# Performance work log

Hardware: AMD Instinct MI355X
Metric: run time of the kernel (lower is better)

Reference implementation:

```python
import jax, jax.numpy as jnp
import numpy as np

N, E, C, L, NG = 50000, 600000, 128, 7, 512
EPS = 1e-7


def layer_norm(z, g, b):
    mu = z.mean(-1, keepdims=True)
    var = ((z - mu) ** 2).mean(-1, keepdims=True)
    return (z - mu) * jax.lax.rsqrt(var + 1e-5) * g + b


def setup_inputs() -> dict:
    key = jax.random.key(0)
    ks = jax.random.split(key, 16)
    inp = {
        'x': jax.random.randint(ks[0], (N, 9), 0, 64, dtype=jnp.int32),
        'edge_index': jax.random.randint(ks[1], (2, E), 0, N, dtype=jnp.int32),
        'edge_attr': jax.random.randint(ks[2], (E, 3), 0, 8, dtype=jnp.int32),
        'batch': jnp.sort(jax.random.randint(ks[3], (N,), 0, NG, dtype=jnp.int32)),
        'atom_emb': jax.random.normal(ks[4], (9, 64, C), jnp.float32) * 0.1,
        'bond_emb': jax.random.normal(ks[5], (3, 8, C), jnp.float32) * 0.1,
        'vn_emb': jnp.zeros((1, C), jnp.float32),
        'conv_W1': jax.random.normal(ks[6], (L, C, 2 * C), jnp.float32) / np.sqrt(C),
        'conv_b1': jnp.zeros((L, 2 * C), jnp.float32),
        'conv_g1': jnp.ones((L, 2 * C), jnp.float32),
        'conv_bb1': jnp.zeros((L, 2 * C), jnp.float32),
        'conv_W2': jax.random.normal(ks[7], (L, 2 * C, C), jnp.float32) / np.sqrt(2 * C),
        'conv_b2': jnp.zeros((L, C), jnp.float32),
        'norm_g': jnp.ones((L, C), jnp.float32),
        'norm_b': jnp.zeros((L, C), jnp.float32),
        'vn_W1': jax.random.normal(ks[8], (L - 1, C, C), jnp.float32) / np.sqrt(C),
        'vn_b1': jnp.zeros((L - 1, C), jnp.float32),
        'vn_g': jnp.ones((L - 1, C), jnp.float32),
        'vn_bb': jnp.zeros((L - 1, C), jnp.float32),
        'vn_W2': jax.random.normal(ks[9], (L - 1, C, C), jnp.float32) / np.sqrt(C),
        'vn_b2': jnp.zeros((L - 1, C), jnp.float32),
    }
    return inp


def reference(x, edge_index, edge_attr, batch, atom_emb, bond_emb, vn_emb,
              conv_W1, conv_b1, conv_g1, conv_bb1, conv_W2, conv_b2,
              norm_g, norm_b, vn_W1, vn_b1, vn_g, vn_bb, vn_W2, vn_b2):
    src, dst = edge_index[0], edge_index[1]

    # AtomEncoder: sum of per-feature embeddings -> [N, C]
    h = atom_emb[jnp.arange(9), x].sum(axis=1)
    # BondEncoder (conv_encode_edge=False) -> [E, C]
    edge_emb = bond_emb[jnp.arange(3), edge_attr].sum(axis=1)

    # virtual node embedding (one per graph)
    vn = jnp.broadcast_to(vn_emb[0], (NG, C))
    h = h + vn[batch]

    def gen_conv(l, hx):
        # GENConv: msg = relu(x_j + e) + eps; softmax aggregation (t=1); MLP(x+m)
        msg = jax.nn.relu(hx[src] + edge_emb) + EPS                      # [E, C]
        mx = jax.ops.segment_max(msg, dst, num_segments=N)               # [N, C]
        e = jnp.exp(msg - mx[dst])
        den = jax.ops.segment_sum(e, dst, num_segments=N)
        m = jax.ops.segment_sum(msg * (e / (den[dst] + 1e-16)), dst, num_segments=N)
        z = hx + m
        z = jax.nn.relu(layer_norm(z @ conv_W1[l] + conv_b1[l], conv_g1[l], conv_bb1[l]))
        return z @ conv_W2[l] + conv_b2[l]

    # res+ block: Conv -> [Norm -> ReLU -> (VN update) -> Conv + res]*
    h = gen_conv(0, h)
    for l in range(1, L):
        h2 = jax.nn.relu(layer_norm(h, norm_g[l - 1], norm_b[l - 1]))
        vtmp = jax.ops.segment_sum(h2, batch, num_segments=NG) + vn
        v = jax.nn.relu(layer_norm(vtmp @ vn_W1[l - 1] + vn_b1[l - 1], vn_g[l - 1], vn_bb[l - 1]))
        vn = v @ vn_W2[l - 1] + vn_b2[l - 1]
        h2 = h2 + vn[batch]
        h = gen_conv(l, h2) + h
    h = layer_norm(h, norm_g[L - 1], norm_b[L - 1])

    # global_add_pool -> [NG, C]
    return jax.ops.segment_sum(h, batch, num_segments=NG)
```

## Files before the change

### kernel.cpp

```cpp
#include <hip/hip_runtime.h>
#include <hip/hip_bf16.h>
#include <stdint.h>

#define N_NODES 50000
#define N_EDGES 600000
#define CH 128
#define NLAYERS 7
#define NGRAPHS 512

typedef __hip_bfloat16 bf16;
using bf16x8 = __attribute__((ext_vector_type(8))) __bf16;
using f32x4  = __attribute__((ext_vector_type(4))) float;
using u32x4  = __attribute__((ext_vector_type(4))) uint32_t;

static __device__ __forceinline__ float b2f(bf16 v){ return __bfloat162float(v); }

static __device__ __forceinline__ void bar_lds(){
  asm volatile("s_waitcnt lgkmcnt(0)" ::: "memory");
  __builtin_amdgcn_sched_barrier(0);
  __builtin_amdgcn_s_barrier();
}

__global__ void k_detect(const uint32_t* __restrict__ g, int* __restrict__ flag){
  if (threadIdx.x == 0 && blockIdx.x == 0) flag[0] = (g[0] == 0x3F803F80u) ? 1 : 0;
}

struct Segs { const void* src[12]; float* dst[12]; int n[12]; };

__global__ void k_cvt_all(const int* __restrict__ flag, Segs S){
  int f = flag[0];
  int seg = blockIdx.y;
  int n = S.n[seg];
  const void* src = S.src[seg];
  float* dst = S.dst[seg];
  for (int i = blockIdx.x*blockDim.x + threadIdx.x; i < n; i += gridDim.x*blockDim.x)
    dst[i] = f ? b2f(((const bf16*)src)[i]) : ((const float*)src)[i];
}

__global__ void k_transpose_all(const int* __restrict__ flag,
    const void* W1, const void* W2, const void* vW1, const void* vW2,
    bf16* W1p, bf16* W2T, bf16* vW1p, bf16* vW2T){
  int f = flag[0];
  const int T0 = NLAYERS*128*256, T1 = NLAYERS*256*128;
  const int T2 = (NLAYERS-1)*128*128;
  int total = T0+T1+2*T2;
  for (int i = blockIdx.x*blockDim.x + threadIdx.x; i < total; i += gridDim.x*blockDim.x){
    float v;
    if (i < T0){
      int idx = i; int l = idx/(128*256); int rem = idx - l*128*256; int k = rem >> 8; int n = rem & 255;
      v = f ? b2f(((const bf16*)W1)[idx]) : ((const float*)W1)[idx];
      W1p[(size_t)l*256*128 + n*128 + (k ^ ((n&7)<<3))] = __float2bfloat16(v);
    } else if (i < T0+T1){
      int idx = i-T0; int l = idx/(256*128); int rem = idx - l*256*128; int k = rem >> 7; int n = rem & 127;
      v = f ? b2f(((const bf16*)W2)[idx]) : ((const float*)W2)[idx];
      W2T[(size_t)l*128*256 + n*256 + k] = __float2bfloat16(v);
    } else if (i < T0+T1+T2){
      int idx = i-T0-T1; int l = idx/(128*128); int rem = idx - l*128*128; int k = rem >> 7; int n = rem & 127;
      v = f ? b2f(((const bf16*)vW1)[idx]) : ((const float*)vW1)[idx];
      vW1p[(size_t)l*128*128 + n*128 + (k ^ ((n&7)<<3))] = __float2bfloat16(v);
    } else {
      int idx = i-T0-T1-T2; int l = idx/(128*128); int rem = idx - l*128*128; int k = rem >> 7; int n = rem & 127;
      v = f ? b2f(((const bf16*)vW2)[idx]) : ((const float*)vW2)[idx];
      vW2T[(size_t)l*128*128 + n*128 + k] = __float2bfloat16(v);
    }
  }
}

__global__ void k_bondC(const int* __restrict__ flag, const void* __restrict__ bond,
                        float* __restrict__ bondC){
  int f = flag[0];
  int i = blockIdx.x*blockDim.x + threadIdx.x;
  if (i >= 512*128) return;
  int idx = i >> 7, c = i & 127;
  int a0 = idx & 7, a1 = (idx>>3) & 7, a2 = (idx>>6) & 7;
  auto g = [&](int e)->float{ return f ? b2f(((const bf16*)bond)[e]) : ((const float*)bond)[e]; };
  bondC[i] = g((0*8+a0)*128 + c) + g((1*8+a1)*128 + c) + g((2*8+a2)*128 + c);
}

__global__ void k_zero_i32(int* p, int n){
  for (int i = blockIdx.x*blockDim.x + threadIdx.x; i < n; i += gridDim.x*blockDim.x) p[i] = 0;
}

__global__ void k_hist(const int* __restrict__ keys, int* __restrict__ counts, int n){
  for (int i = blockIdx.x*blockDim.x + threadIdx.x; i < n; i += gridDim.x*blockDim.x)
    atomicAdd(&counts[keys[i]], 1);
}

__global__ __launch_bounds__(256) void k_scanA(const int* __restrict__ in, int* __restrict__ out,
                                               int* __restrict__ bsums, int n){
  __shared__ int lds[256];
  int t = threadIdx.x;
  int base = blockIdx.x * 1024;
  int v[4]; int s = 0;
  #pragma unroll
  for (int i=0;i<4;i++){ int idx = base + t*4 + i; int x = (idx<n)? in[idx] : 0; v[i]=x; s+=x; }
  lds[t] = s; __syncthreads();
  for (int off=1; off<256; off<<=1){
    int x = (t>=off)? lds[t-off] : 0;
    __syncthreads();
    lds[t] += x;
    __syncthreads();
  }
  int p = lds[t] - s;
  #pragma unroll
  for (int i=0;i<4;i++){ int idx = base + t*4 + i; if (idx<n) out[idx] = p; p += v[i]; }
  if (t==255) bsums[blockIdx.x] = lds[255];
}

__global__ __launch_bounds__(256) void k_scanB(int* bsums, int nblk){
  __shared__ int lds[256];
  int t = threadIdx.x;
  int v = (t<nblk)? bsums[t] : 0;
  lds[t] = v; __syncthreads();
  for (int off=1; off<256; off<<=1){
    int x = (t>=off)? lds[t-off] : 0;
    __syncthreads();
    lds[t] += x;
    __syncthreads();
  }
  if (t<nblk) bsums[t] = lds[t] - v;
}

__global__ void k_scanC(int* out, const int* bsums, int n){
  for (int i = blockIdx.x*blockDim.x + threadIdx.x; i < n; i += gridDim.x*blockDim.x)
    out[i] += bsums[i >> 10];
}

__global__ void k_scatter(const int* __restrict__ ei, const int* __restrict__ ea,
                          const int* __restrict__ row_ptr, int* __restrict__ fill,
                          uint32_t* __restrict__ csr){
  for (int e = blockIdx.x*blockDim.x + threadIdx.x; e < N_EDGES; e += gridDim.x*blockDim.x){
    int src = ei[e];
    int dst = ei[N_EDGES + e];
    int pos = row_ptr[dst] + atomicAdd(&fill[dst], 1);
    uint32_t a0 = (uint32_t)ea[e*3+0], a1 = (uint32_t)ea[e*3+1], a2 = (uint32_t)ea[e*3+2];
    csr[pos] = (uint32_t)src | ((a0 | (a1<<3) | (a2<<6)) << 16);
  }
}

__global__ void k_gptr(const int* __restrict__ batch, int* __restrict__ gptr){
  int i = blockIdx.x*blockDim.x + threadIdx.x;
  if (i >= N_NODES) return;
  int b = batch[i];
  if (i == 0){ for (int g=0; g<=b; ++g) gptr[g] = 0; }
  else { int bp = batch[i-1]; for (int g=bp+1; g<=b; ++g) gptr[g] = i; }
  if (i == N_NODES-1){ for (int g=b+1; g<=NGRAPHS; ++g) gptr[g] = N_NODES; }
}

__global__ __launch_bounds__(128) void k_atom_encode(const int* __restrict__ x,
    const float* __restrict__ atom_emb, const float* __restrict__ vn_emb,
    uint32_t* __restrict__ hxb){
  int n = blockIdx.x; int c = threadIdx.x;
  float s = vn_emb[c];
  #pragma unroll
  for (int f=0; f<9; ++f){
    int xv = x[n*9+f];
    s += atom_emb[(f*64 + xv)*CH + c];
  }
  float o = __shfl_xor(s, 1);
  if ((c & 1) == 0){
    __hip_bfloat162 p; p.x = __float2bfloat16(s); p.y = __float2bfloat16(o);
    hxb[n*64 + (c>>1)] = *reinterpret_cast<uint32_t*>(&p);
  }
}

__global__ void k_vn_init(const float* __restrict__ vn_emb, float* __restrict__ vn){
  for (int i = blockIdx.x*blockDim.x + threadIdx.x; i < NGRAPHS*CH; i += gridDim.x*blockDim.x)
    vn[i] = vn_emb[i & (CH-1)];
}

__global__ __launch_bounds__(256) void k_aggregate(const uint32_t* __restrict__ hxb,
     const uint32_t* __restrict__ csr, const int* __restrict__ row_ptr,
     const float* __restrict__ bondC, uint32_t* __restrict__ z){
  int n = blockIdx.x*4 + (threadIdx.x >> 6);
  int t = threadIdx.x & 63;
  int s0 = row_ptr[n], s1 = row_ptr[n+1];
  float sa=0.f, sb=0.f, wa=0.f, wb=0.f;
  int i = s0;
  for (; i+4 <= s1; i += 4){
    uint32_t u0=csr[i], u1=csr[i+1], u2=csr[i+2], u3=csr[i+3];
    uint32_t h0 = hxb[(size_t)(u0 & 0xFFFFu)*64 + t];
    uint32_t h1 = hxb[(size_t)(u1 & 0xFFFFu)*64 + t];
    uint32_t h2 = hxb[(size_t)(u2 & 0xFFFFu)*64 + t];
    uint32_t h3 = hxb[(size_t)(u3 & 0xFFFFu)*64 + t];
    float2 c0 = *reinterpret_cast<const float2*>(bondC + (size_t)(u0 >> 16)*128 + 2*t);
    float2 c1 = *reinterpret_cast<const float2*>(bondC + (size_t)(u1 >> 16)*128 + 2*t);
    float2 c2 = *reinterpret_cast<const float2*>(bondC + (size_t)(u2 >> 16)*128 + 2*t);
    float2 c3 = *reinterpret_cast<const float2*>(bondC + (size_t)(u3 >> 16)*128 + 2*t);
    #define EDGE(hp, bc) { \
      float va = __uint_as_float(hp << 16) + bc.x; \
      float vb = __uint_as_float(hp & 0xFFFF0000u) + bc.y; \
      va = fmaxf(va, 0.f) + 1e-7f; vb = fmaxf(vb, 0.f) + 1e-7f; \
      float pa = __expf(va - 10.f), pb = __expf(vb - 10.f); \
      sa += pa; wa += pa*va; sb += pb; wb += pb*vb; }
    EDGE(h0, c0) EDGE(h1, c1) EDGE(h2, c2) EDGE(h3, c3)
  }
  for (; i < s1; ++i){
    uint32_t u = csr[i];
    uint32_t hp = hxb[(size_t)(u & 0xFFFFu)*64 + t];
    float2 bc = *reinterpret_cast<const float2*>(bondC + (size_t)(u >> 16)*128 + 2*t);
    EDGE(hp, bc)
    #undef EDGE
  }
  uint32_t own = hxb[(size_t)n*64 + t];
  float za = __uint_as_float(own << 16)         + wa/(sa + 1e-16f);
  float zb = __uint_as_float(own & 0xFFFF0000u) + wb/(sb + 1e-16f);
  __hip_bfloat162 p; p.x = __float2bfloat16(za); p.y = __float2bfloat16(zb);
  z[(size_t)n*64 + (t ^ ((n&7)<<2))] = *reinterpret_cast<uint32_t*>(&p);
}

template<int K, int N1, int N2, bool VNIN>
__global__ __launch_bounds__(512, 4) void k_mlp9(const bf16* __restrict__ A,
    const float* __restrict__ Af32,
    const bf16* __restrict__ W1s,
    const float* __restrict__ b1, const float* __restrict__ g1, const float* __restrict__ bb1,
    const bf16* __restrict__ W2T,
    const float* __restrict__ b2,
    const float* __restrict__ lng, const float* __restrict__ lnb,
    const float* __restrict__ residual, float* __restrict__ out,
    bf16* __restrict__ hxn, int relu2, int M)
{
  constexpr int KK1 = K/32;
  constexpr int WC  = N1/4;
  constexpr int JC  = WC/16;
  constexpr int KK2 = N1/32;
  constexpr int REGA = N1*K*2;
  constexpr int REGB = 64*K*2;
  __shared__ __align__(16) char smem[REGA + REGB];
  bf16* W1L = (bf16*)smem;
  bf16* zt  = (bf16*)smem;
  bf16* AL  = (bf16*)(smem + REGA);
  float* lnp = (float*)(smem + REGA);
  float* lnv = (float*)(smem + REGA + 2048);

  const int tid = threadIdx.x;
  const int wid = tid >> 6, lane = tid & 63;
  const int wr = wid >> 2, wc = wid & 3;
  const int rlo = lane & 15, hi = lane >> 4, khi = hi*8;
  const int t = blockIdx.x;

  #pragma unroll
  for (int c = 0; c < REGA/8192; ++c){
    int cc = c*8 + wid;
    __builtin_amdgcn_global_load_lds((const uint32_t*)((const char*)W1s + cc*1024 + lane*16),
                                     (uint32_t*)(smem + cc*1024), 16, 0, 0);
  }
  if constexpr (!VNIN){
    const char* src = (const char*)A + (size_t)t*REGB;
    #pragma unroll
    for (int c = 0; c < REGB/8192; ++c){
      int cc = c*8 + wid;
      __builtin_amdgcn_global_load_lds((const uint32_t*)(src + cc*1024 + lane*16),
                                       (uint32_t*)((char*)AL + cc*1024), 16, 0, 0);
    }
  } else {
    int base = t*64;
    #pragma unroll
    for (int e=0;e<(64*K/4)/512;++e){
      int idx = tid + e*512;
      int row = idx >> 5;
      int k4  = (idx & 31)*4;
      float4 v = *reinterpret_cast<const float4*>(Af32 + (size_t)(base+row)*K + k4);
      int s = (row&7)<<3;
      bf16* d = &AL[row*K + (k4 ^ s)];
      d[0]=__float2bfloat16(v.x); d[1]=__float2bfloat16(v.y);
      d[2]=__float2bfloat16(v.z); d[3]=__float2bfloat16(v.w);
    }
  }

  float b1v[JC], gv[JC], bbv[JC];
  #pragma unroll
  for (int jc=0;jc<JC;++jc){
    int col = wc*WC + jc*16 + rlo;
    b1v[jc] = b1[col]; gv[jc] = g1[col]; bbv[jc] = bb1[col];
  }
  float bv2[2] = { b2[wc*32 + rlo], b2[wc*32 + 16 + rlo] };
  float lngv[2] = {0.f,0.f}, lnbv[2] = {0.f,0.f};
  if (hxn){
    lngv[0] = lng[wc*32 + rlo];      lnbv[0] = lnb[wc*32 + rlo];
    lngv[1] = lng[wc*32 + 16 + rlo]; lnbv[1] = lnb[wc*32 + 16 + rlo];
  }
  __syncthreads();

  f32x4 acc1[2][JC];
  #pragma unroll
  for (int rt=0;rt<2;++rt)
    #pragma unroll
    for (int jc=0;jc<JC;++jc) acc1[rt][jc] = {0.f,0.f,0.f,0.f};
  #pragma unroll
  for (int kk=0;kk<KK1;++kk){
    bf16x8 af[2], bw[JC];
    #pragma unroll
    for (int rt=0;rt<2;++rt){
      int lr = wr*32 + rt*16 + rlo;
      af[rt] = *reinterpret_cast<const bf16x8*>(&AL[lr*K + ((kk*32 + khi) ^ ((lr&7)<<3))]);
    }
    #pragma unroll
    for (int jc=0;jc<JC;++jc){
      int n = wc*WC + jc*16 + rlo;
      bw[jc] = *reinterpret_cast<const bf16x8*>(&W1L[n*K + ((kk*32 + khi) ^ ((n&7)<<3))]);
    }
    #pragma unroll
    for (int rt=0;rt<2;++rt)
      #pragma unroll
      for (int jc=0;jc<JC;++jc)
        acc1[rt][jc] = __builtin_amdgcn_mfma_f32_16x16x32_bf16(af[rt], bw[jc], acc1[rt][jc], 0,0,0);
  }

  float resv[2][2][4];
  if (residual){
    #pragma unroll
    for (int rt=0;rt<2;++rt)
      #pragma unroll
      for (int r=0;r<4;++r){
        int grow = t*64 + wr*32 + rt*16 + hi*4 + r; if (grow >= M) grow = M-1;
        #pragma unroll
        for (int ct=0;ct<2;++ct)
          resv[rt][ct][r] = residual[(size_t)grow*N2 + wc*32 + ct*16 + rlo];
      }
  }
  __builtin_amdgcn_sched_barrier(0);

  float p[2][4], q[2][4];
  #pragma unroll
  for (int rt=0;rt<2;++rt)
    #pragma unroll
    for (int r=0;r<4;++r){ p[rt][r]=0.f; q[rt][r]=0.f; }
  #pragma unroll
  for (int jc=0;jc<JC;++jc)
    #pragma unroll
    for (int rt=0;rt<2;++rt)
      #pragma unroll
      for (int r=0;r<4;++r){
        float v = acc1[rt][jc][r] + b1v[jc]; acc1[rt][jc][r] = v;
        p[rt][r] += v; q[rt][r] += v*v;
      }
  float pr[2][4], qr[2][4];
  #pragma unroll
  for (int rt=0;rt<2;++rt)
    #pragma unroll
    for (int r=0;r<4;++r){
      float pv = p[rt][r], qv = q[rt][r];
      #pragma unroll
      for (int off=1; off<16; off<<=1){ pv += __shfl_xor(pv, off); qv += __shfl_xor(qv, off); }
      pr[rt][r] = pv; qr[rt][r] = qv;
    }
  bar_lds();

  #pragma unroll
  for (int rt=0;rt<2;++rt)
    #pragma unroll
    for (int r=0;r<4;++r)
      if (rlo == 0){
        int row = wr*32 + rt*16 + hi*4 + r;
        lnp[(row*4 + wc)*2 + 0] = pr[rt][r];
        lnp[(row*4 + wc)*2 + 1] = qr[rt][r];
      }
  bar_lds();
  if (tid < 64){
    float P=0.f, Q=0.f;
    #pragma unroll
    for (int w=0;w<4;++w){ P += lnp[(tid*4+w)*2]; Q += lnp[(tid*4+w)*2+1]; }
    float mu = P*(1.f/N1);
    lnv[tid*2]   = mu;
    lnv[tid*2+1] = rsqrtf(Q*(1.f/N1) - mu*mu + 1e-5f);
  }
  bar_lds();

  #pragma unroll
  for (int rt=0;rt<2;++rt)
    #pragma unroll
    for (int r=0;r<4;++r){
      int row = wr*32 + rt*16 + hi*4 + r;
      float mu = lnv[row*2], rs = lnv[row*2+1];
      #pragma unroll
      for (int jc=0;jc<JC;++jc){
        int col = wc*WC + jc*16 + rlo;
        float y = (acc1[rt][jc][r]-mu)*rs*gv[jc] + bbv[jc];
        zt[row*N1 + (col ^ ((row&7)<<3))] = __float2bfloat16(fmaxf(y, 0.f));
      }
    }
  u32x4 b2raw[2][KK2];
  #pragma unroll
  for (int ct=0;ct<2;++ct){
    const bf16* wp = W2T + (size_t)(wc*32 + ct*16 + rlo)*N1 + khi;
    #pragma unroll
    for (int kk=0;kk<KK2;++kk)
      b2raw[ct][kk] = *reinterpret_cast<const u32x4*>(wp + kk*32);
  }
  bar_lds();

  f32x4 acc2[2][2];
  #pragma unroll
  for (int rt=0;rt<2;++rt)
    #pragma unroll
    for (int ct=0;ct<2;++ct) acc2[rt][ct] = {0.f,0.f,0.f,0.f};
  #pragma unroll
  for (int kk=0;kk<KK2;++kk){
    bf16x8 a2[2];
    #pragma unroll
    for (int rt=0;rt<2;++rt){
      int row = wr*32 + rt*16 + rlo;
      a2[rt] = *reinterpret_cast<const bf16x8*>(&zt[row*N1 + ((kk*32 + khi) ^ ((row&7)<<3))]);
    }
    #pragma unroll
    for (int rt=0;rt<2;++rt)
      #pragma unroll
      for (int ct=0;ct<2;++ct){
        bf16x8 bb;
        __builtin_memcpy(&bb, &b2raw[ct][kk], 16);
        acc2[rt][ct] = __builtin_amdgcn_mfma_f32_16x16x32_bf16(a2[rt], bb, acc2[rt][ct], 0,0,0);
      }
  }

  float vmat[2][2][4];
  #pragma unroll
  for (int rt=0;rt<2;++rt)
    #pragma unroll
    for (int ct=0;ct<2;++ct)
      #pragma unroll
      for (int r=0;r<4;++r){
        float v = acc2[rt][ct][r] + bv2[ct];
        if (residual) v += resv[rt][ct][r];
        vmat[rt][ct][r] = v;
        int grow = t*64 + wr*32 + rt*16 + hi*4 + r;
        if (grow < M) out[(size_t)grow*N2 + wc*32 + ct*16 + rlo] = v;
      }

  if (hxn){
    #pragma unroll
    for (int rt=0;rt<2;++rt)
      #pragma unroll
      for (int r=0;r<4;++r){
        float pv = vmat[rt][0][r] + vmat[rt][1][r];
        float qv = vmat[rt][0][r]*vmat[rt][0][r] + vmat[rt][1][r]*vmat[rt][1][r];
        #pragma unroll
        for (int off=1; off<16; off<<=1){ pv += __shfl_xor(pv, off); qv += __shfl_xor(qv, off); }
        if (rlo == 0){
          int row = wr*32 + rt*16 + hi*4 + r;
          lnp[(row*4 + wc)*2 + 0] = pv;
          lnp[(row*4 + wc)*2 + 1] = qv;
        }
      }
    bar_lds();
    if (tid < 64){
      float P=0.f, Q=0.f;
      #pragma unroll
      for (int w=0;w<4;++w){ P += lnp[(tid*4+w)*2]; Q += lnp[(tid*4+w)*2+1]; }
      float mu = P*(1.f/N2);
      lnv[tid*2]   = mu;
      lnv[tid*2+1] = rsqrtf(Q*(1.f/N2) - mu*mu + 1e-5f);
    }
    bar_lds();
    #pragma unroll
    for (int rt=0;rt<2;++rt)
      #pragma unroll
      for (int r=0;r<4;++r){
        int row = wr*32 + rt*16 + hi*4 + r;
        float mu = lnv[row*2], rs = lnv[row*2+1];
        int grow = t*64 + row;
        if (grow < M){
          #pragma unroll
          for (int ct=0;ct<2;++ct){
            float y = (vmat[rt][ct][r]-mu)*rs*lngv[ct] + lnbv[ct];
            if (relu2) y = fmaxf(y, 0.f);
            hxn[(size_t)grow*N2 + wc*32 + ct*16 + rlo] = __float2bfloat16(y);
          }
        }
      }
  }
}

__global__ void k_vncopy(const float* __restrict__ vn, float* __restrict__ vnacc){
  int i = blockIdx.x*blockDim.x + threadIdx.x;
  if (i < NGRAPHS*CH) vnacc[i] = vn[i];
}

#define SEGC 128
__global__ __launch_bounds__(128) void k_segsum2(const bf16* __restrict__ hxn,
    const int* __restrict__ batch, float* __restrict__ vnacc){
  int c = threadIdx.x;
  int n0 = blockIdx.x*SEGC;
  int n1 = n0 + SEGC; if (n1 > N_NODES) n1 = N_NODES;
  if (n0 >= N_NODES) return;
  int cur = batch[n0];
  float s = 0.f;
  for (int n = n0; n < n1; ++n){
    int b = batch[n];
    if (b != cur){ atomicAdd(&vnacc[cur*CH + c], s); s = 0.f; cur = b; }
    s += b2f(hxn[(size_t)n*CH + c]);
  }
  atomicAdd(&vnacc[cur*CH + c], s);
}

__global__ void k_add_vn(const uint32_t* __restrict__ hxn, const float* __restrict__ vn,
                         const int* __restrict__ batch, uint32_t* __restrict__ hxb){
  for (int i = blockIdx.x*blockDim.x + threadIdx.x; i < N_NODES*64; i += gridDim.x*blockDim.x){
    int n = i >> 6; int t = i & 63;
    uint32_t hp = hxn[i];
    float2 vv = *reinterpret_cast<const float2*>(vn + (size_t)batch[n]*CH + 2*t);
    float za = __uint_as_float(hp << 16)         + vv.x;
    float zb = __uint_as_float(hp & 0xFFFF0000u) + vv.y;
    __hip_bfloat162 p; p.x = __float2bfloat16(za); p.y = __float2bfloat16(zb);
    hxb[i] = *reinterpret_cast<uint32_t*>(&p);
  }
}

__global__ __launch_bounds__(128) void k_pool(const bf16* __restrict__ hxn,
    const int* __restrict__ gptr, const int* __restrict__ flag, void* __restrict__ out){
  int g = blockIdx.x; int c = threadIdx.x;
  float s = 0.f;
  for (int n = gptr[g]; n < gptr[g+1]; ++n) s += b2f(hxn[(size_t)n*CH + c]);
  if (flag[0]) ((bf16*)out)[g*CH+c] = __float2bfloat16(s);
  else         ((float*)out)[g*CH+c] = s;
}

extern "C" void kernel_launch(void* const* d_in, const int* in_sizes, int n_in,
                              void* d_out, int out_size, void* d_ws, size_t ws_size,
                              hipStream_t stream)
{
  const int*  x     = (const int*) d_in[0];
  const int*  ei    = (const int*) d_in[1];
  const int*  ea    = (const int*) d_in[2];
  const int*  batch = (const int*) d_in[3];
  const void* atom_emb = d_in[4];
  const void* bond_emb = d_in[5];
  const void* vn_emb   = d_in[6];
  const void* conv_W1  = d_in[7];
  const void* conv_b1  = d_in[8];
  const void* conv_g1  = d_in[9];
  const void* conv_bb1 = d_in[10];
  const void* conv_W2  = d_in[11];
  const void* conv_b2  = d_in[12];
  const void* norm_g   = d_in[13];
  const void* norm_b   = d_in[14];
  const void* vn_W1    = d_in[15];
  const void* vn_b1    = d_in[16];
  const void* vn_g     = d_in[17];
  const void* vn_bb    = d_in[18];
  const void* vn_W2    = d_in[19];
  const void* vn_b2    = d_in[20];

  char* wsb = (char*)d_ws;
  size_t off = 0;
  auto alloc = [&](size_t bytes)->char*{ char* p = wsb + off; off += (bytes + 255) & ~(size_t)255; return p; };
  const int ZROWS = 50048;
  float*    h     = (float*)   alloc(sizeof(float)*N_NODES*CH);
  uint32_t* hxn   = (uint32_t*)alloc(sizeof(uint32_t)*ZROWS*64);
  uint32_t* hxb   = (uint32_t*)alloc(sizeof(uint32_t)*N_NODES*64);
  uint32_t* z     = (uint32_t*)alloc(sizeof(uint32_t)*ZROWS*64);
  float*    vn    = (float*)   alloc(sizeof(float)*NGRAPHS*CH);
  float*    vnacc = (float*)   alloc(sizeof(float)*NGRAPHS*CH);
  bf16*     W1Tp  = (bf16*)    alloc(sizeof(bf16)*NLAYERS*256*128);
  bf16*     W2T   = (bf16*)    alloc(sizeof(bf16)*NLAYERS*128*256);
  bf16*     vW1Tp = (bf16*)    alloc(sizeof(bf16)*(NLAYERS-1)*128*128);
  bf16*     vW2T  = (bf16*)    alloc(sizeof(bf16)*(NLAYERS-1)*128*128);
  int* row_ptr = (int*)alloc(sizeof(int)*(N_NODES+1));
  int* counts  = (int*)alloc(sizeof(int)*(N_NODES+1));
  uint32_t* csr = (uint32_t*)alloc(sizeof(uint32_t)*N_EDGES);
  int* gptr    = (int*)alloc(sizeof(int)*(NGRAPHS+1));
  int* bsums   = (int*)alloc(sizeof(int)*256);
  int* flag    = (int*)alloc(sizeof(int)*64);
  float* atomF = (float*)alloc(sizeof(float)*9*64*CH);
  float* bondC = (float*)alloc(sizeof(float)*512*CH);
  float* vnEF  = (float*)alloc(sizeof(float)*CH);
  float* b1F   = (float*)alloc(sizeof(float)*NLAYERS*2*CH);
  float* g1F   = (float*)alloc(sizeof(float)*NLAYERS*2*CH);
  float* bb1F  = (float*)alloc(sizeof(float)*NLAYERS*2*CH);
  float* b2F   = (float*)alloc(sizeof(float)*NLAYERS*CH);
  float* ngF   = (float*)alloc(sizeof(float)*NLAYERS*CH);
  float* nbF   = (float*)alloc(sizeof(float)*NLAYERS*CH);
  float* vb1F  = (float*)alloc(sizeof(float)*(NLAYERS-1)*CH);
  float* vgF   = (float*)alloc(sizeof(float)*(NLAYERS-1)*CH);
  float* vbbF  = (float*)alloc(sizeof(float)*(NLAYERS-1)*CH);
  float* vb2F  = (float*)alloc(sizeof(float)*(NLAYERS-1)*CH);

  k_detect<<<1, 64, 0, stream>>>((const uint32_t*)norm_g, flag);
  Segs S;
  int si = 0;
  auto seg = [&](const void* s_, float* d_, int n_){ S.src[si]=s_; S.dst[si]=d_; S.n[si]=n_; ++si; };
  seg(atom_emb, atomF, 9*64*CH);
  seg(vn_emb,   vnEF,  CH);
  seg(conv_b1,  b1F,  NLAYERS*2*CH);
  seg(conv_g1,  g1F,  NLAYERS*2*CH);
  seg(conv_bb1, bb1F, NLAYERS*2*CH);
  seg(conv_b2,  b2F,  NLAYERS*CH);
  seg(norm_g,   ngF,  NLAYERS*CH);
  seg(norm_b,   nbF,  NLAYERS*CH);
  seg(vn_b1,    vb1F, (NLAYERS-1)*CH);
  seg(vn_g,     vgF,  (NLAYERS-1)*CH);
  seg(vn_bb,    vbbF, (NLAYERS-1)*CH);
  seg(vn_b2,    vb2F, (NLAYERS-1)*CH);
  k_cvt_all<<<dim3(72, 12), 256, 0, stream>>>(flag, S);
  k_transpose_all<<<640, 256, 0, stream>>>(flag, conv_W1, conv_W2, vn_W1, vn_W2,
                                           W1Tp, W2T, vW1Tp, vW2T);
  k_bondC<<<256, 256, 0, stream>>>(flag, bond_emb, bondC);

  k_zero_i32<<<64, 256, 0, stream>>>(counts, N_NODES+1);
  k_hist<<<512, 256, 0, stream>>>(ei + N_EDGES, counts, N_EDGES);
  int nblkE = (N_NODES+1 + 1023)/1024;
  k_scanA<<<nblkE, 256, 0, stream>>>(counts, row_ptr, bsums, N_NODES+1);
  k_scanB<<<1, 256, 0, stream>>>(bsums, nblkE);
  k_scanC<<<64, 256, 0, stream>>>(row_ptr, bsums, N_NODES+1);
  k_zero_i32<<<64, 256, 0, stream>>>(counts, N_NODES+1);
  k_scatter<<<512, 256, 0, stream>>>(ei, ea, row_ptr, counts, csr);
  k_gptr<<<(N_NODES+255)/256, 256, 0, stream>>>(batch, gptr);

  k_atom_encode<<<N_NODES, 128, 0, stream>>>(x, atomF, vnEF, hxb);
  k_vn_init<<<64, 256, 0, stream>>>(vnEF, vn);

  const int NT_CONV = (N_NODES + 63)/64;
  const int NT_VN   = NGRAPHS/64;

  for (int l = 0; l < NLAYERS; ++l){
    if (l > 0){
      k_vncopy<<<(NGRAPHS*CH+255)/256, 256, 0, stream>>>(vn, vnacc);
      k_segsum2<<<(N_NODES+SEGC-1)/SEGC, 128, 0, stream>>>((const bf16*)hxn, batch, vnacc);
      k_mlp9<128,128,128,true><<<NT_VN, 512, 0, stream>>>(nullptr, vnacc,
          vW1Tp + (size_t)(l-1)*128*128, vb1F + (l-1)*CH, vgF + (l-1)*CH, vbbF + (l-1)*CH,
          vW2T + (size_t)(l-1)*128*128, vb2F + (l-1)*CH,
          nullptr, nullptr, nullptr, vn, nullptr, 0, NGRAPHS);
      k_add_vn<<<1024, 256, 0, stream>>>(hxn, vn, batch, hxb);
    }
    k_aggregate<<<N_NODES/4, 256, 0, stream>>>(hxb, csr, row_ptr, bondC, z);
    k_mlp9<128,256,128,false><<<NT_CONV, 512, 0, stream>>>((const bf16*)z, nullptr,
        W1Tp + (size_t)l*256*128, b1F + l*2*CH, g1F + l*2*CH, bb1F + l*2*CH,
        W2T + (size_t)l*128*256, b2F + l*CH,
        ngF + l*CH, nbF + l*CH,
        (l==0)? nullptr : h, h, (bf16*)hxn, (l < NLAYERS-1) ? 1 : 0, N_NODES);
  }
  k_pool<<<NGRAPHS, 128, 0, stream>>>((const bf16*)hxn, gptr, flag, d_out);
}
```

Measured before the change: 1.101 ms.

## Pack bond table to bf16, use one-wave aggregate blocks, relax MLP launch bounds

The precomputed bond embedding table is now stored as packed bf16 pairs instead of float, which halves its footprint and the gather bytes per edge in the aggregation kernel. The aggregation kernel now launches one 64-thread block per node instead of four nodes per 256-thread block. The MLP kernel's launch bounds drop from 4 to 2 blocks per SM, and the epilogue reuses the accumulator registers in place of a separate temporary array, presumably to ease register pressure. Bond sums are rounded to bf16, which lowers precision slightly, and the lower occupancy hint could reduce latency hiding.

```diff
diff --git a/kernel.cpp b/kernel.cpp
--- a/kernel.cpp
+++ b/kernel.cpp
@@ -67,14 +67,18 @@
 }
 
 __global__ void k_bondC(const int* __restrict__ flag, const void* __restrict__ bond,
-                        float* __restrict__ bondC){
+                        uint32_t* __restrict__ bondC){
+  int i = blockIdx.x*blockDim.x + threadIdx.x;
+  if (i >= 512*64) return;
   int f = flag[0];
-  int i = blockIdx.x*blockDim.x + threadIdx.x;
-  if (i >= 512*128) return;
-  int idx = i >> 7, c = i & 127;
+  int idx = i >> 6, t = i & 63;
   int a0 = idx & 7, a1 = (idx>>3) & 7, a2 = (idx>>6) & 7;
   auto g = [&](int e)->float{ return f ? b2f(((const bf16*)bond)[e]) : ((const float*)bond)[e]; };
-  bondC[i] = g((0*8+a0)*128 + c) + g((1*8+a1)*128 + c) + g((2*8+a2)*128 + c);
+  int c0 = 2*t, c1 = 2*t+1;
+  float s0 = g((0*8+a0)*128 + c0) + g((1*8+a1)*128 + c0) + g((2*8+a2)*128 + c0);
+  float s1 = g((0*8+a0)*128 + c1) + g((1*8+a1)*128 + c1) + g((2*8+a2)*128 + c1);
+  __hip_bfloat162 p; p.x = __float2bfloat16(s0); p.y = __float2bfloat16(s1);
+  bondC[i] = *reinterpret_cast<uint32_t*>(&p);
 }
 
 __global__ void k_zero_i32(int* p, int n){
@@ -169,11 +173,10 @@
     vn[i] = vn_emb[i & (CH-1)];
 }
 
-__global__ __launch_bounds__(256) void k_aggregate(const uint32_t* __restrict__ hxb,
+__global__ __launch_bounds__(64) void k_aggregate(const uint32_t* __restrict__ hxb,
      const uint32_t* __restrict__ csr, const int* __restrict__ row_ptr,
-     const float* __restrict__ bondC, uint32_t* __restrict__ z){
-  int n = blockIdx.x*4 + (threadIdx.x >> 6);
-  int t = threadIdx.x & 63;
+     const uint32_t* __restrict__ bondC, uint32_t* __restrict__ z){
+  int n = blockIdx.x; int t = threadIdx.x;
   int s0 = row_ptr[n], s1 = row_ptr[n+1];
   float sa=0.f, sb=0.f, wa=0.f, wb=0.f;
   int i = s0;
@@ -183,13 +186,13 @@
     uint32_t h1 = hxb[(size_t)(u1 & 0xFFFFu)*64 + t];
     uint32_t h2 = hxb[(size_t)(u2 & 0xFFFFu)*64 + t];
     uint32_t h3 = hxb[(size_t)(u3 & 0xFFFFu)*64 + t];
-    float2 c0 = *reinterpret_cast<const float2*>(bondC + (size_t)(u0 >> 16)*128 + 2*t);
-    float2 c1 = *reinterpret_cast<const float2*>(bondC + (size_t)(u1 >> 16)*128 + 2*t);
-    float2 c2 = *reinterpret_cast<const float2*>(bondC + (size_t)(u2 >> 16)*128 + 2*t);
-    float2 c3 = *reinterpret_cast<const float2*>(bondC + (size_t)(u3 >> 16)*128 + 2*t);
+    uint32_t c0 = bondC[(size_t)(u0 >> 16)*64 + t];
+    uint32_t c1 = bondC[(size_t)(u1 >> 16)*64 + t];
+    uint32_t c2 = bondC[(size_t)(u2 >> 16)*64 + t];
+    uint32_t c3 = bondC[(size_t)(u3 >> 16)*64 + t];
     #define EDGE(hp, bc) { \
-      float va = __uint_as_float(hp << 16) + bc.x; \
-      float vb = __uint_as_float(hp & 0xFFFF0000u) + bc.y; \
+      float va = __uint_as_float(hp << 16) + __uint_as_float(bc << 16); \
+      float vb = __uint_as_float(hp & 0xFFFF0000u) + __uint_as_float(bc & 0xFFFF0000u); \
       va = fmaxf(va, 0.f) + 1e-7f; vb = fmaxf(vb, 0.f) + 1e-7f; \
       float pa = __expf(va - 10.f), pb = __expf(vb - 10.f); \
       sa += pa; wa += pa*va; sb += pb; wb += pb*vb; }
@@ -198,7 +201,7 @@
   for (; i < s1; ++i){
     uint32_t u = csr[i];
     uint32_t hp = hxb[(size_t)(u & 0xFFFFu)*64 + t];
-    float2 bc = *reinterpret_cast<const float2*>(bondC + (size_t)(u >> 16)*128 + 2*t);
+    uint32_t bc = bondC[(size_t)(u >> 16)*64 + t];
     EDGE(hp, bc)
     #undef EDGE
   }
@@ -210,7 +213,7 @@
 }
 
 template<int K, int N1, int N2, bool VNIN>
-__global__ __launch_bounds__(512, 4) void k_mlp9(const bf16* __restrict__ A,
+__global__ __launch_bounds__(512, 2) void k_mlp10(const bf16* __restrict__ A,
     const float* __restrict__ Af32,
     const bf16* __restrict__ W1s,
     const float* __restrict__ b1, const float* __restrict__ g1, const float* __restrict__ bb1,
@@ -413,7 +416,6 @@
       }
   }
 
-  float vmat[2][2][4];
   #pragma unroll
   for (int rt=0;rt<2;++rt)
     #pragma unroll
@@ -422,7 +424,7 @@
       for (int r=0;r<4;++r){
         float v = acc2[rt][ct][r] + bv2[ct];
         if (residual) v += resv[rt][ct][r];
-        vmat[rt][ct][r] = v;
+        acc2[rt][ct][r] = v;
         int grow = t*64 + wr*32 + rt*16 + hi*4 + r;
         if (grow < M) out[(size_t)grow*N2 + wc*32 + ct*16 + rlo] = v;
       }
@@ -432,8 +434,8 @@
     for (int rt=0;rt<2;++rt)
       #pragma unroll
       for (int r=0;r<4;++r){
-        float pv = vmat[rt][0][r] + vmat[rt][1][r];
-        float qv = vmat[rt][0][r]*vmat[rt][0][r] + vmat[rt][1][r]*vmat[rt][1][r];
+        float pv = acc2[rt][0][r] + acc2[rt][1][r];
+        float qv = acc2[rt][0][r]*acc2[rt][0][r] + acc2[rt][1][r]*acc2[rt][1][r];
         #pragma unroll
         for (int off=1; off<16; off<<=1){ pv += __shfl_xor(pv, off); qv += __shfl_xor(qv, off); }
         if (rlo == 0){
@@ -462,7 +464,7 @@
         if (grow < M){
           #pragma unroll
           for (int ct=0;ct<2;++ct){
-            float y = (vmat[rt][ct][r]-mu)*rs*lngv[ct] + lnbv[ct];
+            float y = (acc2[rt][ct][r]-mu)*rs*lngv[ct] + lnbv[ct];
             if (relu2) y = fmaxf(y, 0.f);
             hxn[(size_t)grow*N2 + wc*32 + ct*16 + rlo] = __float2bfloat16(y);
           }
@@ -562,7 +564,7 @@
   int* bsums   = (int*)alloc(sizeof(int)*256);
   int* flag    = (int*)alloc(sizeof(int)*64);
   float* atomF = (float*)alloc(sizeof(float)*9*64*CH);
-  float* bondC = (float*)alloc(sizeof(float)*512*CH);
+  uint32_t* bondC = (uint32_t*)alloc(sizeof(uint32_t)*512*64);
   float* vnEF  = (float*)alloc(sizeof(float)*CH);
   float* b1F   = (float*)alloc(sizeof(float)*NLAYERS*2*CH);
   float* g1F   = (float*)alloc(sizeof(float)*NLAYERS*2*CH);
@@ -594,7 +596,7 @@
   k_cvt_all<<<dim3(72, 12), 256, 0, stream>>>(flag, S);
   k_transpose_all<<<640, 256, 0, stream>>>(flag, conv_W1, conv_W2, vn_W1, vn_W2,
                                            W1Tp, W2T, vW1Tp, vW2T);
-  k_bondC<<<256, 256, 0, stream>>>(flag, bond_emb, bondC);
+  k_bondC<<<128, 256, 0, stream>>>(flag, bond_emb, bondC);
 
   k_zero_i32<<<64, 256, 0, stream>>>(counts, N_NODES+1);
   k_hist<<<512, 256, 0, stream>>>(ei + N_EDGES, counts, N_EDGES);
@@ -616,14 +618,14 @@
     if (l > 0){
       k_vncopy<<<(NGRAPHS*CH+255)/256, 256, 0, stream>>>(vn, vnacc);
       k_segsum2<<<(N_NODES+SEGC-1)/SEGC, 128, 0, stream>>>((const bf16*)hxn, batch, vnacc);
-      k_mlp9<128,128,128,true><<<NT_VN, 512, 0, stream>>>(nullptr, vnacc,
+      k_mlp10<128,128,128,true><<<NT_VN, 512, 0, stream>>>(nullptr, vnacc,
           vW1Tp + (size_t)(l-1)*128*128, vb1F + (l-1)*CH, vgF + (l-1)*CH, vbbF + (l-1)*CH,
           vW2T + (size_t)(l-1)*128*128, vb2F + (l-1)*CH,
           nullptr, nullptr, nullptr, vn, nullptr, 0, NGRAPHS);
       k_add_vn<<<1024, 256, 0, stream>>>(hxn, vn, batch, hxb);
     }
-    k_aggregate<<<N_NODES/4, 256, 0, stream>>>(hxb, csr, row_ptr, bondC, z);
-    k_mlp9<128,256,128,false><<<NT_CONV, 512, 0, stream>>>((const bf16*)z, nullptr,
+    k_aggregate<<<N_NODES, 64, 0, stream>>>(hxb, csr, row_ptr, bondC, z);
+    k_mlp10<128,256,128,false><<<NT_CONV, 512, 0, stream>>>((const bf16*)z, nullptr,
         W1Tp + (size_t)l*256*128, b1F + l*2*CH, g1F + l*2*CH, bb1F + l*2*CH,
         W2T + (size_t)l*128*256, b2F + l*CH,
         ngF + l*CH, nbF + l*CH,
```

Result: faster. 1.026 ms (-6.8%).
